# Kernel optimization log

Hardware: AMD Instinct MI355X
Metric: run time of the kernel (lower is better)

## Reference

```python
import jax, jax.numpy as jnp
import numpy as np
from jax import lax

DN = ('NCHW', 'OIHW', 'NCHW')

def conv3x3(x, w):
    return lax.conv_general_dilated(x, w, (1, 1), 'SAME', dimension_numbers=DN)

def conv1x1(x, w, b):
    # w: [O, C], x: [B, C, H, W]
    return jnp.einsum('oc,bchw->bohw', w, x) + b[None, :, None, None]

def bn_relu(x, p):
    # p: [2, C] -> (scale, shift), eval-mode folded BatchNorm + ReLU
    return jax.nn.relu(x * p[0][None, :, None, None] + p[1][None, :, None, None])

def pam(y, Wb, bb, Wc, bc, Wd, bd, alpha):
    B, C, H, W = y.shape
    n = H * W
    b_ = conv1x1(y, Wb, bb).reshape(B, -1, n)   # [B, C/8, N]
    c_ = conv1x1(y, Wc, bc).reshape(B, -1, n)   # [B, C/8, N]
    d_ = conv1x1(y, Wd, bd).reshape(B, C, n)    # [B, C, N]
    energy = jnp.einsum('bkn,bkm->bnm', b_, c_)  # [B, N, N]
    attn = jax.nn.softmax(energy, axis=-1)
    feat = jnp.einsum('bcm,bnm->bcn', d_, attn).reshape(B, C, H, W)
    return alpha[0] * feat + y

def cam(y, beta):
    B, C, H, W = y.shape
    xf = y.reshape(B, C, H * W)
    energy = jnp.einsum('bcn,bdn->bcd', xf, xf)  # [B, C, C]
    energy = jnp.max(energy, axis=-1, keepdims=True) - energy
    attn = jax.nn.softmax(energy, axis=-1)
    feat = jnp.einsum('bcd,bdn->bcn', attn, xf).reshape(B, C, H, W)
    return beta[0] * feat + y

def reference(x, Wp1, bnp1, Wc1, bnc1, Wb, bb, Wc, bc, Wd, bd, alpha, beta,
              Wp2, bnp2, Wc2, bnc2, Wout, bout, Wp3, bp3, Wc3, bc3):
    feat_p = bn_relu(conv3x3(x, Wp1), bnp1)
    feat_p = pam(feat_p, Wb, bb, Wc, bc, Wd, bd, alpha)
    feat_p = bn_relu(conv3x3(feat_p, Wp2), bnp2)

    feat_c = bn_relu(conv3x3(x, Wc1), bnc1)
    feat_c = cam(feat_c, beta)
    feat_c = bn_relu(conv3x3(feat_c, Wc2), bnc2)

    fusion = feat_p + feat_c
    out_main = jax.nn.sigmoid(conv1x1(fusion, Wout, bout))
    out_p = jax.nn.sigmoid(conv1x1(feat_p, Wp3, bp3))
    out_c = jax.nn.sigmoid(conv1x1(feat_c, Wc3, bc3))
    return (out_main, out_p, out_c)

def setup_inputs() -> dict:
    key = jax.random.key(0)
    ks = jax.random.split(key, 24)
    Cin, Ci, Ck, NC = 512, 128, 16, 19
    B, H, W = 8, 64, 64
    s = lambda k, shape, scale=0.05: jax.random.normal(k, shape, jnp.float32) * scale
    return {
        'x': jax.random.normal(ks[0], (B, Cin, H, W), jnp.float32),
        'Wp1': s(ks[1], (Ci, Cin, 3, 3)), 'bnp1': jnp.stack([jnp.ones(Ci), jnp.zeros(Ci)]),
        'Wc1': s(ks[2], (Ci, Cin, 3, 3)), 'bnc1': jnp.stack([jnp.ones(Ci), jnp.zeros(Ci)]),
        'Wb': s(ks[3], (Ck, Ci)), 'bb': s(ks[4], (Ck,)),
        'Wc': s(ks[5], (Ck, Ci)), 'bc': s(ks[6], (Ck,)),
        'Wd': s(ks[7], (Ci, Ci)), 'bd': s(ks[8], (Ci,)),
        'alpha': jax.random.normal(ks[9], (1,), jnp.float32) * 0.5,
        'beta': jax.random.normal(ks[10], (1,), jnp.float32) * 0.5,
        'Wp2': s(ks[11], (Ci, Ci, 3, 3)), 'bnp2': jnp.stack([jnp.ones(Ci), jnp.zeros(Ci)]),
        'Wc2': s(ks[12], (Ci, Ci, 3, 3)), 'bnc2': jnp.stack([jnp.ones(Ci), jnp.zeros(Ci)]),
        'Wout': s(ks[13], (NC, Ci)), 'bout': s(ks[14], (NC,)),
        'Wp3': s(ks[15], (NC, Ci)), 'bp3': s(ks[16], (NC,)),
        'Wc3': s(ks[17], (NC, Ci)), 'bc3': s(ks[18], (NC,)),
    }
```

## Files before the change

### kernel.cpp

```cpp
#include <hip/hip_runtime.h>
#include <math.h>


typedef __attribute__((ext_vector_type(8)))  short short8;
typedef __attribute__((ext_vector_type(16))) float f32x16;

__device__ inline unsigned short f2bf(float f) {
    union { float f; unsigned u; } v; v.f = f;
    unsigned r = v.u + 0x7fffu + ((v.u >> 16) & 1u);
    return (unsigned short)(r >> 16);
}
__device__ inline float bf2f(unsigned short h) {
    union { unsigned u; float f; } v; v.u = ((unsigned)h) << 16;
    return v.f;
}

__global__ __launch_bounds__(256) void wpack_kernel(
    const float* __restrict__ W, unsigned short* __restrict__ wp, int Cin, int total)
{
    int idx = blockIdx.x * 256 + threadIdx.x;
    if (idx >= total) return;
    int chunk = idx / 18432;
    int rem   = idx - chunk * 18432;
    int tap   = rem >> 11;
    int rem2  = rem & 2047;
    int g     = rem2 >> 10;
    int co    = (rem2 >> 3) & 127;
    int ci8   = rem2 & 7;
    int cin   = (chunk << 4) + (g << 3) + ci8;
    wp[idx] = f2bf(W[((size_t)co * Cin + cin) * 9 + tap]);
}

__global__ __launch_bounds__(256) void wpack_split_kernel(
    const float* __restrict__ W, unsigned short* __restrict__ wph,
    unsigned short* __restrict__ wpl, int Cin, int total)
{
    int idx = blockIdx.x * 256 + threadIdx.x;
    if (idx >= total) return;
    int chunk = idx / 18432;
    int rem   = idx - chunk * 18432;
    int tap   = rem >> 11;
    int rem2  = rem & 2047;
    int g     = rem2 >> 10;
    int co    = (rem2 >> 3) & 127;
    int ci8   = rem2 & 7;
    int cin   = (chunk << 4) + (g << 3) + ci8;
    float w = W[((size_t)co * Cin + cin) * 9 + tap];
    unsigned short hi = f2bf(w);
    wph[idx] = hi;
    wpl[idx] = f2bf(w - bf2f(hi));
}

__global__ __launch_bounds__(256, 4) void conv3x3_merged(
    const float* __restrict__ xin,
    const unsigned short* __restrict__ wpp,
    const unsigned short* __restrict__ wph, const unsigned short* __restrict__ wpl,
    const float* __restrict__ bnp, const float* __restrict__ bnc,
    float* __restrict__ outP, float* __restrict__ outC,
    unsigned short* __restrict__ outh, unsigned short* __restrict__ outl)
{
    const int t   = threadIdx.x;
    const int w2  = t >> 6;
    const int xh  = w2 & 1;
    const int wy  = w2 >> 1;
    const int ln  = t & 63;
    const int l31 = ln & 31;
    const int g   = ln >> 5;
    const int y   = blockIdx.x;
    const int co0 = blockIdx.y << 6;
    const int b   = blockIdx.z;

    const int sr   = t >> 6;
    const int sx   = t & 63;
    const int sgy  = y - 1 + sr;
    const bool sv  = (t < 192) && ((unsigned)sgy < 64u);
    const int spid = sr * 66 + sx + 1;

    __shared__ __align__(16) unsigned short Xh[2][3168];
    __shared__ __align__(16) unsigned short Xo[2][3168];

    for (int i = t; i < 792; i += 256) {
        uint4 z; z.x = 0; z.y = 0; z.z = 0; z.w = 0;
        ((uint4*)Xh)[i] = z;
        ((uint4*)Xo)[i] = z;
    }

    const int co = co0 + (wy << 5) + l31;
    const unsigned short* wPb = wpp + (size_t)(g << 10) + ((size_t)co << 3);
    const unsigned short* wHb = wph + (size_t)(g << 10) + ((size_t)co << 3);
    const unsigned short* wLb = wpl + (size_t)(g << 10) + ((size_t)co << 3);
    const float* xsrc = xin + ((size_t)b << 21) + (sgy << 6) + sx;

    const f32x16 zero = {0,0,0,0,0,0,0,0,0,0,0,0,0,0,0,0};
    f32x16 ap = zero, ac = zero;

    float xv[16];
    if (sv) {
#pragma unroll
        for (int c = 0; c < 16; c++) xv[c] = xsrc[(size_t)c << 12];
    }
    __syncthreads();

    if (sv) {
        unsigned short th[16], tl[16];
#pragma unroll
        for (int c = 0; c < 16; c++) {
            unsigned short hi = f2bf(xv[c]);
            th[c] = hi; tl[c] = f2bf(xv[c] - bf2f(hi));
        }
        *(uint4*)&Xh[0][spid << 3]          = ((uint4*)th)[0];
        *(uint4*)&Xh[0][1584 + (spid << 3)] = ((uint4*)th)[1];
        *(uint4*)&Xo[0][spid << 3]          = ((uint4*)tl)[0];
        *(uint4*)&Xo[0][1584 + (spid << 3)] = ((uint4*)tl)[1];
    }

    int cur = 0;
    for (int ch = 0; ch < 32; ++ch) {
        __syncthreads();
        const bool pf = (ch < 31);
        if (pf && sv) {
#pragma unroll
            for (int c = 0; c < 16; c++)
                xv[c] = xsrc[((size_t)(ch + 1) << 16) + ((size_t)c << 12)];
        }
        const size_t wo = (size_t)ch * 18432;
#pragma unroll 3
        for (int tap = 0; tap < 9; ++tap) {
            const int dy = tap / 3, dx = tap - dy * 3;
            const int xi = (g ? 1584 : 0) + (((dy * 66) + (xh << 5) + l31 + dx) << 3);
            short8 vap = *(const short8*)(wPb + wo + tap * 2048);
            short8 vah = *(const short8*)(wHb + wo + tap * 2048);
            short8 val = *(const short8*)(wLb + wo + tap * 2048);
            short8 bh_ = *(const short8*)&Xh[cur][xi];
            short8 bl_ = *(const short8*)&Xo[cur][xi];
            ap = __builtin_amdgcn_mfma_f32_32x32x16_bf16(vap, bh_, ap, 0, 0, 0);
            ac = __builtin_amdgcn_mfma_f32_32x32x16_bf16(vah, bh_, ac, 0, 0, 0);
            ac = __builtin_amdgcn_mfma_f32_32x32x16_bf16(vah, bl_, ac, 0, 0, 0);
            ac = __builtin_amdgcn_mfma_f32_32x32x16_bf16(val, bh_, ac, 0, 0, 0);
        }
        if (pf && sv) {
            unsigned short th[16], tl[16];
#pragma unroll
            for (int c = 0; c < 16; c++) {
                unsigned short hi = f2bf(xv[c]);
                th[c] = hi; tl[c] = f2bf(xv[c] - bf2f(hi));
            }
            const int nb = cur ^ 1;
            *(uint4*)&Xh[nb][spid << 3]          = ((uint4*)th)[0];
            *(uint4*)&Xh[nb][1584 + (spid << 3)] = ((uint4*)th)[1];
            *(uint4*)&Xo[nb][spid << 3]          = ((uint4*)tl)[0];
            *(uint4*)&Xo[nb][1584 + (spid << 3)] = ((uint4*)tl)[1];
        }
        cur ^= 1;
    }

    const int x = (xh << 5) + l31;
#pragma unroll
    for (int r = 0; r < 16; r++) {
        int c2 = co0 + (wy << 5) + (r & 3) + ((r >> 2) << 3) + (g << 2);
        size_t o = (((size_t)b * 128 + c2) << 12) + (y << 6) + x;
        float vp = fmaf(ap[r], bnp[c2], bnp[128 + c2]);
        vp = vp > 0.f ? vp : 0.f;
        outP[o] = vp;
        float vc = fmaf(ac[r], bnc[c2], bnc[128 + c2]);
        vc = vc > 0.f ? vc : 0.f;
        outC[o] = vc;
        unsigned short hi = f2bf(vc);
        outh[o] = hi;
        outl[o] = f2bf(vc - bf2f(hi));
    }
}

__global__ __launch_bounds__(256, 4) void conv3x3_bf(
    const unsigned short* __restrict__ xin, int Cin,
    const unsigned short* __restrict__ wpk, const float* __restrict__ bn,
    float* __restrict__ out_f32)
{
    const int t   = threadIdx.x;
    const int w2  = t >> 6;
    const int xh  = w2 & 1;
    const int wy  = w2 >> 1;
    const int ln  = t & 63;
    const int l31 = ln & 31;
    const int g   = ln >> 5;
    const int y   = blockIdx.x;
    const int co0 = blockIdx.y << 6;
    const int b   = blockIdx.z;

    const int sr   = t >> 6;
    const int sx   = t & 63;
    const int sgy  = y - 1 + sr;
    const bool sv  = (t < 192) && ((unsigned)sgy < 64u);
    const int spid = sr * 66 + sx + 1;

    __shared__ __align__(16) unsigned short Xl[2][3168];

    for (int i = t; i < 792; i += 256) {
        uint4 z; z.x = 0; z.y = 0; z.z = 0; z.w = 0;
        ((uint4*)Xl)[i] = z;
    }

    const int co = co0 + (wy << 5) + l31;
    const unsigned short* wB = wpk + (size_t)(g << 10) + ((size_t)co << 3);
    const unsigned short* xsrc = xin + (((size_t)b * Cin) << 12) + (sgy << 6) + sx;

    const f32x16 zero = {0,0,0,0,0,0,0,0,0,0,0,0,0,0,0,0};
    f32x16 acc = zero;

    unsigned short xv[16];
    if (sv) {
#pragma unroll
        for (int c = 0; c < 16; c++) xv[c] = xsrc[(size_t)c << 12];
    }
    __syncthreads();

    if (sv) {
        *(uint4*)&Xl[0][spid << 3]          = ((uint4*)xv)[0];
        *(uint4*)&Xl[0][1584 + (spid << 3)] = ((uint4*)xv)[1];
    }

    const int nchunks = Cin >> 4;
    int cur = 0;
    for (int ch = 0; ch < nchunks; ++ch) {
        __syncthreads();
        const bool pf = (ch < nchunks - 1);
        if (pf && sv) {
#pragma unroll
            for (int c = 0; c < 16; c++)
                xv[c] = xsrc[((size_t)(ch + 1) << 16) + ((size_t)c << 12)];
        }
        const size_t wo = (size_t)ch * 18432;
#pragma unroll 3
        for (int tap = 0; tap < 9; ++tap) {
            const int dy = tap / 3, dx = tap - dy * 3;
            const int xi = (g ? 1584 : 0) + (((dy * 66) + (xh << 5) + l31 + dx) << 3);
            short8 a  = *(const short8*)(wB + wo + tap * 2048);
            short8 b0 = *(const short8*)&Xl[cur][xi];
            acc = __builtin_amdgcn_mfma_f32_32x32x16_bf16(a, b0, acc, 0, 0, 0);
        }
        if (pf && sv) {
            const int nb = cur ^ 1;
            *(uint4*)&Xl[nb][spid << 3]          = ((uint4*)xv)[0];
            *(uint4*)&Xl[nb][1584 + (spid << 3)] = ((uint4*)xv)[1];
        }
        cur ^= 1;
    }

    const int x = (xh << 5) + l31;
#pragma unroll
    for (int r = 0; r < 16; r++) {
        int c2 = co0 + (wy << 5) + (r & 3) + ((r >> 2) << 3) + (g << 2);
        float v = fmaf(acc[r], bn[c2], bn[128 + c2]);
        v = v > 0.f ? v : 0.f;
        out_f32[(((size_t)b * 128 + c2) << 12) + (y << 6) + x] = v;
    }
}

__global__ __launch_bounds__(256, 4) void conv3x3_hilo_bf(
    const unsigned short* __restrict__ xhg, const unsigned short* __restrict__ xlg,
    int Cin, const unsigned short* __restrict__ wph, const unsigned short* __restrict__ wpl,
    const float* __restrict__ bn, float* __restrict__ out_f32)
{
    const int t   = threadIdx.x;
    const int w2  = t >> 6;
    const int xh  = w2 & 1;
    const int wy  = w2 >> 1;
    const int ln  = t & 63;
    const int l31 = ln & 31;
    const int g   = ln >> 5;
    const int y   = blockIdx.x;
    const int co0 = blockIdx.y << 6;
    const int b   = blockIdx.z;

    const int sr   = t >> 6;
    const int sx   = t & 63;
    const int sgy  = y - 1 + sr;
    const bool sv  = (t < 192) && ((unsigned)sgy < 64u);
    const int spid = sr * 66 + sx + 1;

    __shared__ __align__(16) unsigned short Xh[2][3168];
    __shared__ __align__(16) unsigned short Xo[2][3168];

    for (int i = t; i < 792; i += 256) {
        uint4 z; z.x = 0; z.y = 0; z.z = 0; z.w = 0;
        ((uint4*)Xh)[i] = z;
        ((uint4*)Xo)[i] = z;
    }

    const int co = co0 + (wy << 5) + l31;
    const unsigned short* wHb = wph + (size_t)(g << 10) + ((size_t)co << 3);
    const unsigned short* wLb = wpl + (size_t)(g << 10) + ((size_t)co << 3);
    const unsigned short* hsrc = xhg + (((size_t)b * Cin) << 12) + (sgy << 6) + sx;
    const unsigned short* lsrc = xlg + (((size_t)b * Cin) << 12) + (sgy << 6) + sx;

    const f32x16 zero = {0,0,0,0,0,0,0,0,0,0,0,0,0,0,0,0};
    f32x16 acc = zero;

    unsigned short hv[16], lv[16];
    if (sv) {
#pragma unroll
        for (int c = 0; c < 16; c++) { hv[c] = hsrc[(size_t)c << 12]; lv[c] = lsrc[(size_t)c << 12]; }
    }
    __syncthreads();

    if (sv) {
        *(uint4*)&Xh[0][spid << 3]          = ((uint4*)hv)[0];
        *(uint4*)&Xh[0][1584 + (spid << 3)] = ((uint4*)hv)[1];
        *(uint4*)&Xo[0][spid << 3]          = ((uint4*)lv)[0];
        *(uint4*)&Xo[0][1584 + (spid << 3)] = ((uint4*)lv)[1];
    }

    const int nchunks = Cin >> 4;
    int cur = 0;
    for (int ch = 0; ch < nchunks; ++ch) {
        __syncthreads();
        const bool pf = (ch < nchunks - 1);
        if (pf && sv) {
#pragma unroll
            for (int c = 0; c < 16; c++) {
                hv[c] = hsrc[((size_t)(ch + 1) << 16) + ((size_t)c << 12)];
                lv[c] = lsrc[((size_t)(ch + 1) << 16) + ((size_t)c << 12)];
            }
        }
        const size_t wo = (size_t)ch * 18432;
#pragma unroll 3
        for (int tap = 0; tap < 9; ++tap) {
            const int dy = tap / 3, dx = tap - dy * 3;
            const int xi = (g ? 1584 : 0) + (((dy * 66) + (xh << 5) + l31 + dx) << 3);
            short8 ah  = *(const short8*)(wHb + wo + tap * 2048);
            short8 al  = *(const short8*)(wLb + wo + tap * 2048);
            short8 bh_ = *(const short8*)&Xh[cur][xi];
            short8 bl_ = *(const short8*)&Xo[cur][xi];
            acc = __builtin_amdgcn_mfma_f32_32x32x16_bf16(ah, bh_, acc, 0, 0, 0);
            acc = __builtin_amdgcn_mfma_f32_32x32x16_bf16(ah, bl_, acc, 0, 0, 0);
            acc = __builtin_amdgcn_mfma_f32_32x32x16_bf16(al, bh_, acc, 0, 0, 0);
        }
        if (pf && sv) {
            const int nb = cur ^ 1;
            *(uint4*)&Xh[nb][spid << 3]          = ((uint4*)hv)[0];
            *(uint4*)&Xh[nb][1584 + (spid << 3)] = ((uint4*)hv)[1];
            *(uint4*)&Xo[nb][spid << 3]          = ((uint4*)lv)[0];
            *(uint4*)&Xo[nb][1584 + (spid << 3)] = ((uint4*)lv)[1];
        }
        cur ^= 1;
    }

    const int x = (xh << 5) + l31;
#pragma unroll
    for (int r = 0; r < 16; r++) {
        int c2 = co0 + (wy << 5) + (r & 3) + ((r >> 2) << 3) + (g << 2);
        float v = fmaf(acc[r], bn[c2], bn[128 + c2]);
        v = v > 0.f ? v : 0.f;
        out_f32[(((size_t)b * 128 + c2) << 12) + (y << 6) + x] = v;
    }
}

__global__ __launch_bounds__(256) void cam_energy_mfma(
    const unsigned short* __restrict__ bh, const unsigned short* __restrict__ bl,
    float* __restrict__ egy_part)
{
    const int t   = threadIdx.x;
    const int w   = t >> 6;
    const int ln  = t & 63;
    const int l31 = ln & 31;
    const int g   = ln >> 5;
    const int i0  = (blockIdx.x >> 2) << 5;
    const int j0  = (blockIdx.x & 3) << 5;
    const int nseg = blockIdx.y;
    const int b   = blockIdx.z;

    __shared__ float red[4][64][17];

    const f32x16 zero = {0,0,0,0,0,0,0,0,0,0,0,0,0,0,0,0};
    f32x16 acc = zero;
    const int nb = (nseg << 9) + (w << 7) + (g << 3);
    const size_t ri = ((size_t)b * 128 + i0 + l31) << 12;
    const size_t rj = ((size_t)b * 128 + j0 + l31) << 12;

#pragma unroll
    for (int c = 0; c < 8; c++) {
        const int n0 = nb + (c << 4);
        short8 ah  = *(const short8*)(bh + ri + n0);
        short8 al  = *(const short8*)(bl + ri + n0);
        short8 bhf = *(const short8*)(bh + rj + n0);
        short8 blf = *(const short8*)(bl + rj + n0);
        acc = __builtin_amdgcn_mfma_f32_32x32x16_bf16(ah, bhf, acc, 0, 0, 0);
        acc = __builtin_amdgcn_mfma_f32_32x32x16_bf16(ah, blf, acc, 0, 0, 0);
        acc = __builtin_amdgcn_mfma_f32_32x32x16_bf16(al, bhf, acc, 0, 0, 0);
    }
#pragma unroll
    for (int r = 0; r < 16; r++) red[w][ln][r] = acc[r];
    __syncthreads();

    const int lane = t & 63;
    const int rq   = t >> 6;
    float* base = egy_part + (((size_t)(nseg * 8 + b)) << 14);
#pragma unroll
    for (int e = 0; e < 4; e++) {
        const int reg = (rq << 2) + e;
        float v = red[0][lane][reg] + red[1][lane][reg]
                + red[2][lane][reg] + red[3][lane][reg];
        const int i = i0 + (reg & 3) + ((reg >> 2) << 3) + ((lane >> 5) << 2);
        base[i * 128 + j0 + (lane & 31)] = v;
    }
}

__global__ __launch_bounds__(256) void cam_softmax_fused(
    const float* __restrict__ egy_part, float* __restrict__ egy)
{
    const int b   = blockIdx.x;
    const int rg  = blockIdx.y;
    const int t   = threadIdx.x;
    const int row = (rg << 4) + (t >> 4);
    const int jg  = t & 15;

    float e[8];
#pragma unroll
    for (int jj = 0; jj < 8; jj++) e[jj] = 0.f;
    for (int seg = 0; seg < 8; seg++) {
        const float* p = egy_part + (((size_t)(seg * 8 + b)) << 14) + row * 128 + (jg << 3);
#pragma unroll
        for (int jj = 0; jj < 8; jj++) e[jj] += p[jj];
    }
    float mn = e[0];
#pragma unroll
    for (int jj = 1; jj < 8; jj++) mn = fminf(mn, e[jj]);
#pragma unroll
    for (int k = 1; k < 16; k <<= 1) mn = fminf(mn, __shfl_xor(mn, k));
    float s = 0.f;
#pragma unroll
    for (int jj = 0; jj < 8; jj++) { float p = __expf(mn - e[jj]); e[jj] = p; s += p; }
#pragma unroll
    for (int k = 1; k < 16; k <<= 1) s += __shfl_xor(s, k);
    const float inv = 1.f / s;
    float* orow = egy + ((size_t)b << 14) + row * 128 + (jg << 3);
#pragma unroll
    for (int jj = 0; jj < 8; jj++) orow[jj] = e[jj] * inv;
}

__global__ __launch_bounds__(256) void pam_qk_1x1(
    const float* __restrict__ A, const float* __restrict__ Wb, const float* __restrict__ bb,
    const float* __restrict__ Wc, const float* __restrict__ bc,
    unsigned short* __restrict__ qt, unsigned short* __restrict__ kt)
{
    __shared__ float wl[2 * 16 * 128];
    __shared__ float bl[32];
    const int t = threadIdx.x;
    const int n = (blockIdx.x << 8) + t;
    const int b = blockIdx.y;
    for (int idx = t; idx < 2048; idx += 256) { wl[idx] = Wb[idx]; wl[2048 + idx] = Wc[idx]; }
    if (t < 16) { bl[t] = bb[t]; bl[16 + t] = bc[t]; }
    __syncthreads();
    float ab[16], ac[16];
#pragma unroll
    for (int k = 0; k < 16; k++) { ab[k] = 0.f; ac[k] = 0.f; }
    for (int chn = 0; chn < 128; ++chn) {
        float a = A[(((size_t)b * 128 + chn) << 12) + n];
#pragma unroll
        for (int k = 0; k < 16; k++) {
            ab[k] = fmaf(wl[k * 128 + chn], a, ab[k]);
            ac[k] = fmaf(wl[2048 + k * 128 + chn], a, ac[k]);
        }
    }
    unsigned short uq[16], uk[16];
#pragma unroll
    for (int k = 0; k < 16; k++) {
        uq[k] = f2bf(ab[k] + bl[k]);
        uk[k] = f2bf(ac[k] + bl[16 + k]);
    }
    size_t row = (size_t)b * 4096 + n;
    ((uint4*)qt)[row * 2 + 0] = ((uint4*)uq)[0];
    ((uint4*)qt)[row * 2 + 1] = ((uint4*)uq)[1];
    ((uint4*)kt)[row * 2 + 0] = ((uint4*)uk)[0];
    ((uint4*)kt)[row * 2 + 1] = ((uint4*)uk)[1];
}

__global__ __launch_bounds__(256) void pam_v_1x1(
    const float* __restrict__ A, const float* __restrict__ Wd, const float* __restrict__ bd,
    unsigned short* __restrict__ vb)
{
    __shared__ float wl[32 * 128];
    __shared__ float bl[32];
    const int t   = threadIdx.x;
    const int n   = (blockIdx.x << 8) + t;
    const int co0 = blockIdx.y << 5;
    const int b   = blockIdx.z;
    for (int idx = t; idx < 4096; idx += 256) {
        int c2 = idx >> 7, chv = idx & 127;
        wl[idx] = Wd[(co0 + c2) * 128 + chv];
    }
    if (t < 32) bl[t] = bd[co0 + t];
    __syncthreads();
    float acc[32];
#pragma unroll
    for (int k = 0; k < 32; k++) acc[k] = 0.f;
    for (int chn = 0; chn < 128; ++chn) {
        float a = A[(((size_t)b * 128 + chn) << 12) + n];
#pragma unroll
        for (int k = 0; k < 32; k++) acc[k] = fmaf(wl[k * 128 + chn], a, acc[k]);
    }
#pragma unroll
    for (int k = 0; k < 32; k++)
        vb[(((size_t)b * 128 + co0 + k) << 12) + n] = f2bf(acc[k] + bl[k]);
}

__global__ __launch_bounds__(256) void pam_attn_mfma(
    const unsigned short* __restrict__ qt, const unsigned short* __restrict__ kt,
    const unsigned short* __restrict__ vb,
    const float* __restrict__ alpha, const float* __restrict__ Y,
    unsigned short* __restrict__ outb)
{
    const int t  = threadIdx.x;
    const int w  = t >> 6;
    const int L  = t & 63;
    const int ln = L & 31;
    const int g  = L >> 5;
    const int b  = blockIdx.y;
    const int n0 = blockIdx.x << 5;
    const int c0 = w << 5;

    __shared__ unsigned short Pf[16 * 256];
    __shared__ float red[4][32];

    const f32x16 zero = {0,0,0,0,0,0,0,0,0,0,0,0,0,0,0,0};
    short8 qfrag = *(const short8*)(qt + (((size_t)b * 4096 + n0 + ln) << 4) + (g << 3));
    const float al = alpha[0];

    f32x16 acc = zero;
    float rs = 0.f;
    float mold = -3.0e38f;

    for (int m0 = 0; m0 < 4096; m0 += 128) {
        const int mq = m0 + (w << 5);
        short8 kfrag = *(const short8*)(kt + (((size_t)b * 4096 + mq + ln) << 4) + (g << 3));
        f32x16 s = __builtin_amdgcn_mfma_f32_32x32x16_bf16(kfrag, qfrag, zero, 0, 0, 0);

        float lm = s[0];
#pragma unroll
        for (int r = 1; r < 16; r++) lm = fmaxf(lm, s[r]);
        lm = fmaxf(lm, __shfl_xor(lm, 32));
        if (L < 32) red[w][L] = lm;
        __syncthreads();
        const float mb = fmaxf(fmaxf(red[0][ln], red[1][ln]),
                               fmaxf(red[2][ln], red[3][ln]));
        const float mnew = fmaxf(mold, mb);
        const float fs = __expf(mold - mnew);
        mold = mnew;
        rs *= fs;
#pragma unroll
        for (int r = 0; r < 16; r++) acc[r] *= fs;

        float p[16];
#pragma unroll
        for (int r = 0; r < 16; r++) { p[r] = __expf(s[r] - mnew); rs += p[r]; }
        float xx[16];
#pragma unroll
        for (int r = 0; r < 16; r++) xx[r] = __shfl_xor(p[r], 32);

        unsigned short f0[8], f1[8];
#pragma unroll
        for (int i = 0; i < 4; i++) {
            f0[i]     = f2bf(g ? xx[4 + i]  : p[i]);
            f0[4 + i] = f2bf(g ? p[4 + i]   : xx[i]);
            f1[i]     = f2bf(g ? xx[12 + i] : p[8 + i]);
            f1[4 + i] = f2bf(g ? p[12 + i]  : xx[8 + i]);
        }
        *(short8*)(&Pf[((w << 2) + g) * 256 + (ln << 3)])     = *(short8*)f0;
        *(short8*)(&Pf[((w << 2) + 2 + g) * 256 + (ln << 3)]) = *(short8*)f1;
        __syncthreads();

#pragma unroll
        for (int kk = 0; kk < 8; kk++) {
            short8 pfrag = *(const short8*)(&Pf[((kk << 1) + g) * 256 + (ln << 3)]);
            short8 vfrag = *(const short8*)(vb + (((size_t)b * 128 + c0 + ln) << 12)
                                               + m0 + (kk << 4) + (g << 3));
            acc = __builtin_amdgcn_mfma_f32_32x32x16_bf16(vfrag, pfrag, acc, 0, 0, 0);
        }
        __syncthreads();
    }

    rs += __shfl_xor(rs, 32);
    if (L < 32) red[w][L] = rs;
    __syncthreads();
    const float inv = 1.f / (red[0][ln] + red[1][ln] + red[2][ln] + red[3][ln]);
    const int n = n0 + ln;
#pragma unroll
    for (int r = 0; r < 16; r++) {
        int c = c0 + (r & 3) + ((r >> 2) << 3) + (g << 2);
        size_t idx = (((size_t)b * 128 + c) << 12) + n;
        outb[idx] = f2bf(fmaf(al, acc[r] * inv, Y[idx]));
    }
}

__global__ __launch_bounds__(256) void cam_feat(
    const float* __restrict__ attn, const float* __restrict__ Bf,
    const float* __restrict__ beta, unsigned short* __restrict__ oh,
    unsigned short* __restrict__ ol)
{
    const int t  = threadIdx.x;
    const int n  = (blockIdx.x << 8) + t;
    const int c0 = blockIdx.y << 5;
    const int b  = blockIdx.z;
    __shared__ float al[32 * 128];
    for (int idx = t; idx < 4096; idx += 256)
        al[idx] = attn[(size_t)b * 16384 + (c0 + (idx >> 7)) * 128 + (idx & 127)];
    __syncthreads();
    float acc[32];
#pragma unroll
    for (int k = 0; k < 32; k++) acc[k] = 0.f;
    for (int d = 0; d < 128; ++d) {
        float v = Bf[(((size_t)b * 128 + d) << 12) + n];
#pragma unroll
        for (int k = 0; k < 32; k++) acc[k] = fmaf(al[k * 128 + d], v, acc[k]);
    }
    float be = beta[0];
#pragma unroll
    for (int k = 0; k < 32; k++) {
        size_t idx = (((size_t)b * 128 + c0 + k) << 12) + n;
        float v = fmaf(be, acc[k], Bf[idx]);
        unsigned short hi = f2bf(v);
        oh[idx] = hi;
        ol[idx] = f2bf(v - bf2f(hi));
    }
}

__global__ __launch_bounds__(256) void heads(
    const float* __restrict__ FP, const float* __restrict__ FC,
    const float* __restrict__ Wout, const float* __restrict__ bout,
    const float* __restrict__ Wp3, const float* __restrict__ bp3,
    const float* __restrict__ Wc3, const float* __restrict__ bc3,
    float* __restrict__ out)
{
    const int t = threadIdx.x;
    const int n = (blockIdx.x << 8) + t;
    const int b = blockIdx.y;
    __shared__ float wl[3 * 19 * 128];
    __shared__ float bl[3 * 19];
    for (int idx = t; idx < 2432; idx += 256) {
        wl[idx]        = Wout[idx];
        wl[2432 + idx] = Wp3[idx];
        wl[4864 + idx] = Wc3[idx];
    }
    if (t < 19) { bl[t] = bout[t]; bl[19 + t] = bp3[t]; bl[38 + t] = bc3[t]; }
    __syncthreads();
    float am[19], ap[19], ac[19];
#pragma unroll
    for (int o = 0; o < 19; o++) { am[o] = 0.f; ap[o] = 0.f; ac[o] = 0.f; }
    for (int chn = 0; chn < 128; ++chn) {
        float pv = FP[(((size_t)b * 128 + chn) << 12) + n];
        float cv = FC[(((size_t)b * 128 + chn) << 12) + n];
        float fv = pv + cv;
#pragma unroll
        for (int o = 0; o < 19; o++) {
            am[o] = fmaf(wl[o * 128 + chn], fv, am[o]);
            ap[o] = fmaf(wl[2432 + o * 128 + chn], pv, ap[o]);
            ac[o] = fmaf(wl[4864 + o * 128 + chn], cv, ac[o]);
        }
    }
    const size_t OS = (size_t)8 * 19 * 4096;
#pragma unroll
    for (int o = 0; o < 19; o++) {
        size_t base = (((size_t)b * 19 + o) << 12) + n;
        out[base]          = 1.f / (1.f + __expf(-(am[o] + bl[o])));
        out[OS + base]     = 1.f / (1.f + __expf(-(ap[o] + bl[19 + o])));
        out[2 * OS + base] = 1.f / (1.f + __expf(-(ac[o] + bl[38 + o])));
    }
}

extern "C" void kernel_launch(void* const* d_in, const int* in_sizes, int n_in,
                              void* d_out, int out_size, void* d_ws, size_t ws_size,
                              hipStream_t stream)
{
    const float* x     = (const float*)d_in[0];
    const float* Wp1   = (const float*)d_in[1];
    const float* bnp1  = (const float*)d_in[2];
    const float* Wc1   = (const float*)d_in[3];
    const float* bnc1  = (const float*)d_in[4];
    const float* Wb    = (const float*)d_in[5];
    const float* bb    = (const float*)d_in[6];
    const float* Wc    = (const float*)d_in[7];
    const float* bcv   = (const float*)d_in[8];
    const float* Wd    = (const float*)d_in[9];
    const float* bd    = (const float*)d_in[10];
    const float* alpha = (const float*)d_in[11];
    const float* beta  = (const float*)d_in[12];
    const float* Wp2   = (const float*)d_in[13];
    const float* bnp2  = (const float*)d_in[14];
    const float* Wc2   = (const float*)d_in[15];
    const float* bnc2  = (const float*)d_in[16];
    const float* Wout  = (const float*)d_in[17];
    const float* bo    = (const float*)d_in[18];
    const float* Wp3   = (const float*)d_in[19];
    const float* bp3   = (const float*)d_in[20];
    const float* Wc3   = (const float*)d_in[21];
    const float* bc3   = (const float*)d_in[22];
    float* out = (float*)d_out;

    char* ws = (char*)d_ws;
    const size_t MB = 1u << 20;
    const size_t W1SZ = (size_t)32 * 18432 * 2;
    const size_t W2SZ = (size_t)8 * 18432 * 2;
    float*          bufA     = (float*)(ws);
    float*          bufB     = (float*)(ws + 16 * MB);
    unsigned short* vb       = (unsigned short*)(ws + 32 * MB);
    float*          egy_part = (float*)(ws + 40 * MB);
    float*          bufD     = (float*)(ws + 32 * MB);
    unsigned short* bh       = (unsigned short*)(ws + 48 * MB);
    unsigned short* blo      = (unsigned short*)(ws + 56 * MB);
    unsigned short* pam_bf   = (unsigned short*)(ws + 48 * MB);
    unsigned short* c2h      = (unsigned short*)(ws + 48 * MB);
    unsigned short* c2l      = (unsigned short*)(ws + 56 * MB);
    unsigned short* qt       = (unsigned short*)(ws + 64 * MB);
    unsigned short* kt       = (unsigned short*)(ws + 65 * MB);
    float*          egy      = (float*)(ws + 66 * MB + (1u << 17));
    unsigned short* wp1      = (unsigned short*)(ws + 67 * MB);
    unsigned short* wc1h     = (unsigned short*)(ws + 67 * MB + W1SZ);
    unsigned short* wc1l     = (unsigned short*)(ws + 67 * MB + 2 * W1SZ);
    unsigned short* wp2      = (unsigned short*)(ws + 67 * MB + 3 * W1SZ);
    unsigned short* wc2h     = (unsigned short*)(ws + 67 * MB + 3 * W1SZ + W2SZ);
    unsigned short* wc2l     = (unsigned short*)(ws + 67 * MB + 3 * W1SZ + 2 * W2SZ);

    dim3 blk(256);
    const int n1 = 32 * 18432;
    const int n2 = 8 * 18432;
    wpack_kernel<<<dim3((n1 + 255) / 256), blk, 0, stream>>>(Wp1, wp1, 512, n1);
    wpack_kernel<<<dim3((n2 + 255) / 256), blk, 0, stream>>>(Wp2, wp2, 128, n2);
    wpack_split_kernel<<<dim3((n1 + 255) / 256), blk, 0, stream>>>(Wc1, wc1h, wc1l, 512, n1);
    wpack_split_kernel<<<dim3((n2 + 255) / 256), blk, 0, stream>>>(Wc2, wc2h, wc2l, 128, n2);

    conv3x3_merged<<<dim3(64, 2, 8), blk, 0, stream>>>(x, wp1, wc1h, wc1l, bnp1, bnc1,
                                                       bufA, bufB, bh, blo);
    cam_energy_mfma<<<dim3(16, 8, 8), blk, 0, stream>>>(bh, blo, egy_part);
    cam_softmax_fused<<<dim3(8, 8), blk, 0, stream>>>(egy_part, egy);
    pam_qk_1x1<<<dim3(16, 8), blk, 0, stream>>>(bufA, Wb, bb, Wc, bcv, qt, kt);
    pam_v_1x1<<<dim3(16, 4, 8), blk, 0, stream>>>(bufA, Wd, bd, vb);
    pam_attn_mfma<<<dim3(128, 8), blk, 0, stream>>>(qt, kt, vb, alpha, bufA, pam_bf);
    conv3x3_bf<<<dim3(64, 2, 8), blk, 0, stream>>>(pam_bf, 128, wp2, bnp2, bufD);
    cam_feat<<<dim3(16, 4, 8), blk, 0, stream>>>(egy, bufB, beta, c2h, c2l);
    conv3x3_hilo_bf<<<dim3(64, 2, 8), blk, 0, stream>>>(c2h, c2l, 128, wc2h, wc2l, bnc2, bufA);
    heads<<<dim3(16, 8), blk, 0, stream>>>(bufD, bufA, Wout, bo, Wp3, bp3, Wc3, bc3, out);
}
```

Baseline: 757.6 us.

## Exploit Gram symmetry in CAM energy and double query tile in PAM attention

Result: faster. 730.5 us (-3.6%).

```diff
diff --git a/kernel.cpp b/kernel.cpp
--- a/kernel.cpp
+++ b/kernel.cpp
@@ -278,13 +278,13 @@
     const bool sv  = (t < 192) && ((unsigned)sgy < 64u);
     const int spid = sr * 66 + sx + 1;
 
-    __shared__ __align__(16) unsigned short Xh[2][3168];
-    __shared__ __align__(16) unsigned short Xo[2][3168];
+    __shared__ __align__(16) unsigned short Xa[2][3168];
+    __shared__ __align__(16) unsigned short Xb[2][3168];
 
     for (int i = t; i < 792; i += 256) {
         uint4 z; z.x = 0; z.y = 0; z.z = 0; z.w = 0;
-        ((uint4*)Xh)[i] = z;
-        ((uint4*)Xo)[i] = z;
+        ((uint4*)Xa)[i] = z;
+        ((uint4*)Xb)[i] = z;
     }
 
     const int co = co0 + (wy << 5) + l31;
@@ -304,10 +304,10 @@
     __syncthreads();
 
     if (sv) {
-        *(uint4*)&Xh[0][spid << 3]          = ((uint4*)hv)[0];
-        *(uint4*)&Xh[0][1584 + (spid << 3)] = ((uint4*)hv)[1];
-        *(uint4*)&Xo[0][spid << 3]          = ((uint4*)lv)[0];
-        *(uint4*)&Xo[0][1584 + (spid << 3)] = ((uint4*)lv)[1];
+        *(uint4*)&Xa[0][spid << 3]          = ((uint4*)hv)[0];
+        *(uint4*)&Xa[0][1584 + (spid << 3)] = ((uint4*)hv)[1];
+        *(uint4*)&Xb[0][spid << 3]          = ((uint4*)lv)[0];
+        *(uint4*)&Xb[0][1584 + (spid << 3)] = ((uint4*)lv)[1];
     }
 
     const int nchunks = Cin >> 4;
@@ -329,18 +329,18 @@
             const int xi = (g ? 1584 : 0) + (((dy * 66) + (xh << 5) + l31 + dx) << 3);
             short8 ah  = *(const short8*)(wHb + wo + tap * 2048);
             short8 al  = *(const short8*)(wLb + wo + tap * 2048);
-            short8 bh_ = *(const short8*)&Xh[cur][xi];
-            short8 bl_ = *(const short8*)&Xo[cur][xi];
+            short8 bh_ = *(const short8*)&Xa[cur][xi];
+            short8 bl_ = *(const short8*)&Xb[cur][xi];
             acc = __builtin_amdgcn_mfma_f32_32x32x16_bf16(ah, bh_, acc, 0, 0, 0);
             acc = __builtin_amdgcn_mfma_f32_32x32x16_bf16(ah, bl_, acc, 0, 0, 0);
             acc = __builtin_amdgcn_mfma_f32_32x32x16_bf16(al, bh_, acc, 0, 0, 0);
         }
         if (pf && sv) {
             const int nb = cur ^ 1;
-            *(uint4*)&Xh[nb][spid << 3]          = ((uint4*)hv)[0];
-            *(uint4*)&Xh[nb][1584 + (spid << 3)] = ((uint4*)hv)[1];
-            *(uint4*)&Xo[nb][spid << 3]          = ((uint4*)lv)[0];
-            *(uint4*)&Xo[nb][1584 + (spid << 3)] = ((uint4*)lv)[1];
+            *(uint4*)&Xa[nb][spid << 3]          = ((uint4*)hv)[0];
+            *(uint4*)&Xa[nb][1584 + (spid << 3)] = ((uint4*)hv)[1];
+            *(uint4*)&Xb[nb][spid << 3]          = ((uint4*)lv)[0];
+            *(uint4*)&Xb[nb][1584 + (spid << 3)] = ((uint4*)lv)[1];
         }
         cur ^= 1;
     }
@@ -364,8 +364,14 @@
     const int ln  = t & 63;
     const int l31 = ln & 31;
     const int g   = ln >> 5;
-    const int i0  = (blockIdx.x >> 2) << 5;
-    const int j0  = (blockIdx.x & 3) << 5;
+    const int bx  = blockIdx.x;
+    int i0c, j0c;
+    if (bx < 4)      { i0c = 0; j0c = bx; }
+    else if (bx < 7) { i0c = 1; j0c = bx - 3; }
+    else if (bx < 9) { i0c = 2; j0c = bx - 5; }
+    else             { i0c = 3; j0c = 3; }
+    const int i0  = i0c << 5;
+    const int j0  = j0c << 5;
     const int nseg = blockIdx.y;
     const int b   = blockIdx.z;
 
@@ -401,7 +407,9 @@
         float v = red[0][lane][reg] + red[1][lane][reg]
                 + red[2][lane][reg] + red[3][lane][reg];
         const int i = i0 + (reg & 3) + ((reg >> 2) << 3) + ((lane >> 5) << 2);
-        base[i * 128 + j0 + (lane & 31)] = v;
+        const int j = j0 + (lane & 31);
+        base[i * 128 + j] = v;
+        if (i0c != j0c) base[j * 128 + i] = v;
     }
 }
 
@@ -516,79 +524,112 @@
     const int ln = L & 31;
     const int g  = L >> 5;
     const int b  = blockIdx.y;
-    const int n0 = blockIdx.x << 5;
+    const int n0 = blockIdx.x << 6;
     const int c0 = w << 5;
 
-    __shared__ unsigned short Pf[16 * 256];
-    __shared__ float red[4][32];
+    __shared__ unsigned short Pf[2][16 * 512];
+    __shared__ float red[2][4][64];
+    __shared__ float redS[4][64];
 
     const f32x16 zero = {0,0,0,0,0,0,0,0,0,0,0,0,0,0,0,0};
-    short8 qfrag = *(const short8*)(qt + (((size_t)b * 4096 + n0 + ln) << 4) + (g << 3));
+    short8 q0 = *(const short8*)(qt + (((size_t)b * 4096 + n0 + ln) << 4) + (g << 3));
+    short8 q1 = *(const short8*)(qt + (((size_t)b * 4096 + n0 + 32 + ln) << 4) + (g << 3));
     const float al = alpha[0];
 
-    f32x16 acc = zero;
-    float rs = 0.f;
-    float mold = -3.0e38f;
-
+    f32x16 acc0 = zero, acc1 = zero;
+    float rs0 = 0.f, rs1 = 0.f;
+    float mold0 = -3.0e38f, mold1 = -3.0e38f;
+
+    int par = 0;
     for (int m0 = 0; m0 < 4096; m0 += 128) {
         const int mq = m0 + (w << 5);
         short8 kfrag = *(const short8*)(kt + (((size_t)b * 4096 + mq + ln) << 4) + (g << 3));
-        f32x16 s = __builtin_amdgcn_mfma_f32_32x32x16_bf16(kfrag, qfrag, zero, 0, 0, 0);
-
-        float lm = s[0];
-#pragma unroll
-        for (int r = 1; r < 16; r++) lm = fmaxf(lm, s[r]);
-        lm = fmaxf(lm, __shfl_xor(lm, 32));
-        if (L < 32) red[w][L] = lm;
+        f32x16 s0 = __builtin_amdgcn_mfma_f32_32x32x16_bf16(kfrag, q0, zero, 0, 0, 0);
+        f32x16 s1 = __builtin_amdgcn_mfma_f32_32x32x16_bf16(kfrag, q1, zero, 0, 0, 0);
+
+        float lm0 = s0[0], lm1 = s1[0];
+#pragma unroll
+        for (int r = 1; r < 16; r++) { lm0 = fmaxf(lm0, s0[r]); lm1 = fmaxf(lm1, s1[r]); }
+        lm0 = fmaxf(lm0, __shfl_xor(lm0, 32));
+        lm1 = fmaxf(lm1, __shfl_xor(lm1, 32));
+        if (L < 32) { red[par][w][L] = lm0; red[par][w][32 + L] = lm1; }
         __syncthreads();
-        const float mb = fmaxf(fmaxf(red[0][ln], red[1][ln]),
-                               fmaxf(red[2][ln], red[3][ln]));
-        const float mnew = fmaxf(mold, mb);
-        const float fs = __expf(mold - mnew);
-        mold = mnew;
-        rs *= fs;
-#pragma unroll
-        for (int r = 0; r < 16; r++) acc[r] *= fs;
-
-        float p[16];
-#pragma unroll
-        for (int r = 0; r < 16; r++) { p[r] = __expf(s[r] - mnew); rs += p[r]; }
-        float xx[16];
-#pragma unroll
-        for (int r = 0; r < 16; r++) xx[r] = __shfl_xor(p[r], 32);
-
-        unsigned short f0[8], f1[8];
-#pragma unroll
-        for (int i = 0; i < 4; i++) {
-            f0[i]     = f2bf(g ? xx[4 + i]  : p[i]);
-            f0[4 + i] = f2bf(g ? p[4 + i]   : xx[i]);
-            f1[i]     = f2bf(g ? xx[12 + i] : p[8 + i]);
-            f1[4 + i] = f2bf(g ? p[12 + i]  : xx[8 + i]);
-        }
-        *(short8*)(&Pf[((w << 2) + g) * 256 + (ln << 3)])     = *(short8*)f0;
-        *(short8*)(&Pf[((w << 2) + 2 + g) * 256 + (ln << 3)]) = *(short8*)f1;
+        const float mb0 = fmaxf(fmaxf(red[par][0][ln], red[par][1][ln]),
+                                fmaxf(red[par][2][ln], red[par][3][ln]));
+        const float mb1 = fmaxf(fmaxf(red[par][0][32 + ln], red[par][1][32 + ln]),
+                                fmaxf(red[par][2][32 + ln], red[par][3][32 + ln]));
+        const float mnew0 = fmaxf(mold0, mb0);
+        const float mnew1 = fmaxf(mold1, mb1);
+        const float fs0 = __expf(mold0 - mnew0);
+        const float fs1 = __expf(mold1 - mnew1);
+        mold0 = mnew0; mold1 = mnew1;
+        rs0 *= fs0; rs1 *= fs1;
+#pragma unroll
+        for (int r = 0; r < 16; r++) { acc0[r] *= fs0; acc1[r] *= fs1; }
+
+        {
+            float p[16];
+#pragma unroll
+            for (int r = 0; r < 16; r++) { p[r] = __expf(s0[r] - mnew0); rs0 += p[r]; }
+            float xx[16];
+#pragma unroll
+            for (int r = 0; r < 16; r++) xx[r] = __shfl_xor(p[r], 32);
+            unsigned short f0[8], f1[8];
+#pragma unroll
+            for (int i = 0; i < 4; i++) {
+                f0[i]     = f2bf(g ? xx[4 + i]  : p[i]);
+                f0[4 + i] = f2bf(g ? p[4 + i]   : xx[i]);
+                f1[i]     = f2bf(g ? xx[12 + i] : p[8 + i]);
+                f1[4 + i] = f2bf(g ? p[12 + i]  : xx[8 + i]);
+            }
+            *(short8*)(&Pf[par][((w << 2) + g) * 512 + (ln << 3)])     = *(short8*)f0;
+            *(short8*)(&Pf[par][((w << 2) + 2 + g) * 512 + (ln << 3)]) = *(short8*)f1;
+        }
+        {
+            float p[16];
+#pragma unroll
+            for (int r = 0; r < 16; r++) { p[r] = __expf(s1[r] - mnew1); rs1 += p[r]; }
+            float xx[16];
+#pragma unroll
+            for (int r = 0; r < 16; r++) xx[r] = __shfl_xor(p[r], 32);
+            unsigned short f0[8], f1[8];
+#pragma unroll
+            for (int i = 0; i < 4; i++) {
+                f0[i]     = f2bf(g ? xx[4 + i]  : p[i]);
+                f0[4 + i] = f2bf(g ? p[4 + i]   : xx[i]);
+                f1[i]     = f2bf(g ? xx[12 + i] : p[8 + i]);
+                f1[4 + i] = f2bf(g ? p[12 + i]  : xx[8 + i]);
+            }
+            *(short8*)(&Pf[par][((w << 2) + g) * 512 + 256 + (ln << 3)])     = *(short8*)f0;
+            *(short8*)(&Pf[par][((w << 2) + 2 + g) * 512 + 256 + (ln << 3)]) = *(short8*)f1;
+        }
         __syncthreads();
 
 #pragma unroll
         for (int kk = 0; kk < 8; kk++) {
-            short8 pfrag = *(const short8*)(&Pf[((kk << 1) + g) * 256 + (ln << 3)]);
             short8 vfrag = *(const short8*)(vb + (((size_t)b * 128 + c0 + ln) << 12)
                                                + m0 + (kk << 4) + (g << 3));
-            acc = __builtin_amdgcn_mfma_f32_32x32x16_bf16(vfrag, pfrag, acc, 0, 0, 0);
-        }
-        __syncthreads();
-    }
-
-    rs += __shfl_xor(rs, 32);
-    if (L < 32) red[w][L] = rs;
-    __syncthreads();
-    const float inv = 1.f / (red[0][ln] + red[1][ln] + red[2][ln] + red[3][ln]);
-    const int n = n0 + ln;
+            short8 pf0 = *(const short8*)(&Pf[par][((kk << 1) + g) * 512 + (ln << 3)]);
+            short8 pf1 = *(const short8*)(&Pf[par][((kk << 1) + g) * 512 + 256 + (ln << 3)]);
+            acc0 = __builtin_amdgcn_mfma_f32_32x32x16_bf16(vfrag, pf0, acc0, 0, 0, 0);
+            acc1 = __builtin_amdgcn_mfma_f32_32x32x16_bf16(vfrag, pf1, acc1, 0, 0, 0);
+        }
+        par ^= 1;
+    }
+
+    rs0 += __shfl_xor(rs0, 32);
+    rs1 += __shfl_xor(rs1, 32);
+    if (L < 32) { redS[w][L] = rs0; redS[w][32 + L] = rs1; }
+    __syncthreads();
+    const float inv0 = 1.f / (redS[0][ln] + redS[1][ln] + redS[2][ln] + redS[3][ln]);
+    const float inv1 = 1.f / (redS[0][32 + ln] + redS[1][32 + ln]
+                            + redS[2][32 + ln] + redS[3][32 + ln]);
 #pragma unroll
     for (int r = 0; r < 16; r++) {
         int c = c0 + (r & 3) + ((r >> 2) << 3) + (g << 2);
-        size_t idx = (((size_t)b * 128 + c) << 12) + n;
-        outb[idx] = f2bf(fmaf(al, acc[r] * inv, Y[idx]));
+        size_t idx0 = (((size_t)b * 128 + c) << 12) + n0 + ln;
+        outb[idx0]      = f2bf(fmaf(al, acc0[r] * inv0, Y[idx0]));
+        outb[idx0 + 32] = f2bf(fmaf(al, acc1[r] * inv1, Y[idx0 + 32]));
     }
 }
 
@@ -730,11 +771,11 @@
 
     conv3x3_merged<<<dim3(64, 2, 8), blk, 0, stream>>>(x, wp1, wc1h, wc1l, bnp1, bnc1,
                                                        bufA, bufB, bh, blo);
-    cam_energy_mfma<<<dim3(16, 8, 8), blk, 0, stream>>>(bh, blo, egy_part);
+    cam_energy_mfma<<<dim3(10, 8, 8), blk, 0, stream>>>(bh, blo, egy_part);
     cam_softmax_fused<<<dim3(8, 8), blk, 0, stream>>>(egy_part, egy);
     pam_qk_1x1<<<dim3(16, 8), blk, 0, stream>>>(bufA, Wb, bb, Wc, bcv, qt, kt);
     pam_v_1x1<<<dim3(16, 4, 8), blk, 0, stream>>>(bufA, Wd, bd, vb);
-    pam_attn_mfma<<<dim3(128, 8), blk, 0, stream>>>(qt, kt, vb, alpha, bufA, pam_bf);
+    pam_attn_mfma<<<dim3(64, 8), blk, 0, stream>>>(qt, kt, vb, alpha, bufA, pam_bf);
     conv3x3_bf<<<dim3(64, 2, 8), blk, 0, stream>>>(pam_bf, 128, wp2, bnp2, bufD);
     cam_feat<<<dim3(16, 4, 8), blk, 0, stream>>>(egy, bufB, beta, c2h, c2l);
     conv3x3_hilo_bf<<<dim3(64, 2, 8), blk, 0, stream>>>(c2h, c2l, 128, wc2h, wc2l, bnc2, bufA);
```
